# Optimization experiments

Hardware: AMD Instinct MI355X
Metric: run time of the kernel (lower is better)

The kernel has to match this reference:

```python
import jax, jax.numpy as jnp
import numpy as np

B, S, H = 32, 512, 768
NHEAD, DH = 8, 96          # 8 heads * 96 = 768
E = 4096                   # edges per sample
NC = 2
NEG = -1e9
EPS = 1e-5


def _p(k, shape, scale=0.02):
    return scale * jax.random.normal(k, shape, dtype=jnp.float32)


def setup_inputs() -> dict:
    key = jax.random.key(0)
    ks = jax.random.split(key, 24)
    z = lambda *s: jnp.zeros(s, jnp.float32)
    return {
        "diff_encoded": jax.random.normal(ks[0], (B, S, H), jnp.float32),
        "msg_encoded": jax.random.normal(ks[1], (B, S, H), jnp.float32),
        "msg_mask": jnp.ones((B, S), jnp.int32),
        "edge_index_diff": jax.random.randint(ks[2], (B, 2, E), 0, S),
        "edge_index_msg": jax.random.randint(ks[3], (B, 2, E), 0, S),
        # GATv2Conv(heads=1): lin_l (source/message), lin_r (target), att vector, output bias
        "gat_wl": _p(ks[4], (H, H)), "gat_bl": z(H),
        "gat_wr": _p(ks[5], (H, H)), "gat_br": z(H),
        "gat_att": _p(ks[6], (H,)), "gat_bias": z(H),
        # cross MultiheadAttention
        "wq": _p(ks[7], (H, H)), "bq": z(H),
        "wk": _p(ks[8], (H, H)), "bk": z(H),
        "wv": _p(ks[9], (H, H)), "bv": z(H),
        "wo": _p(ks[10], (H, H)), "bo": z(H),
        # LayerNorm + MLP head
        "ln_g": jnp.ones((H,), jnp.float32), "ln_b": z(H),
        "fc0_w": _p(ks[11], (H, 512)), "fc0_b": z(512),
        "fc1_w": _p(ks[12], (512, 128)), "fc1_b": z(128),
        "fc2_w": _p(ks[13], (128, NC)), "fc2_b": z(NC),
    }


def _gat_single(x, edges, wl, bl, wr, br, att, bias):
    # GATv2Conv, heads=1, add_self_loops=True. x: [N,H], edges: [2,E] (src, dst).
    N = x.shape[0]
    src, dst = edges[0], edges[1]
    valid = (src < N) & (dst < N)            # clip_edge_index, as a mask
    src = jnp.where(valid, src, 0)
    dst = jnp.where(valid, dst, 0)
    loop = jnp.arange(N, dtype=src.dtype)    # PyG adds self loops
    src_a = jnp.concatenate([src, loop])
    dst_a = jnp.concatenate([dst, loop])
    valid_a = jnp.concatenate([valid, jnp.ones((N,), bool)])
    xl = x @ wl + bl                          # source / message transform
    xr = x @ wr + br                          # target transform
    e = jax.nn.leaky_relu(xl[src_a] + xr[dst_a], 0.2) @ att   # [E+N]
    e = jnp.where(valid_a, e, NEG)
    emax = jax.ops.segment_max(e, dst_a, num_segments=N)
    p = jnp.exp(e - emax[dst_a]) * valid_a.astype(x.dtype)
    denom = jax.ops.segment_sum(p, dst_a, num_segments=N)
    alpha = p / denom[dst_a]
    out = jax.ops.segment_sum(alpha[:, None] * xl[src_a], dst_a, num_segments=N)
    return out + bias


_gat = jax.vmap(_gat_single, in_axes=(0, 0) + (None,) * 6)


def _layernorm(x, g, b):
    mu = jnp.mean(x, -1, keepdims=True)
    var = jnp.mean(jnp.square(x - mu), -1, keepdims=True)
    return (x - mu) * jax.lax.rsqrt(var + EPS) * g + b


def reference(diff_encoded, msg_encoded, msg_mask, edge_index_diff, edge_index_msg,
              gat_wl, gat_bl, gat_wr, gat_br, gat_att, gat_bias,
              wq, bq, wk, bk, wv, bv, wo, bo, ln_g, ln_b,
              fc0_w, fc0_b, fc1_w, fc1_b, fc2_w, fc2_b):
    diff_g = _gat(diff_encoded, edge_index_diff, gat_wl, gat_bl, gat_wr, gat_br, gat_att, gat_bias) + diff_encoded
    msg_g = _gat(msg_encoded, edge_index_msg, gat_wl, gat_bl, gat_wr, gat_br, gat_att, gat_bias) + msg_encoded
    # cross attention: query=diff_g, key/value=msg_g, key_padding_mask = (msg_mask == 0)
    q = (diff_g @ wq + bq).reshape(B, S, NHEAD, DH)
    k = (msg_g @ wk + bk).reshape(B, S, NHEAD, DH)
    v = (msg_g @ wv + bv).reshape(B, S, NHEAD, DH)
    scores = jnp.einsum("bqhd,bkhd->bhqk", q, k) / jnp.sqrt(jnp.float32(DH))
    scores = jnp.where((msg_mask == 0)[:, None, None, :], NEG, scores)
    attn = jax.nn.softmax(scores, axis=-1)
    ctx = jnp.einsum("bhqk,bkhd->bqhd", attn, v).reshape(B, S, H) @ wo + bo
    fused = _layernorm(ctx + diff_g, ln_g, ln_b)
    x = fused[:, 0, :]                                  # CLS token
    x = jax.nn.relu(x @ fc0_w + fc0_b)                  # dropout = identity (eval)
    x = jax.nn.relu(x @ fc1_w + fc1_b)
    return x @ fc2_w + fc2_b
```

## Files before the change

### kernel.cpp

```cpp
#include <hip/hip_runtime.h>
#include <hip/hip_bf16.h>
#include <math.h>

#define BB 32
#define SS 512
#define HH 768
#define NHEADC 8
#define DHC 96
#define EE 4096
#define NCC 2
#define CAPC 128
#define CAP2 32
#define GSL 36
#define NEGV -1000000000.0f
#define EPSV 1e-5f

#define PREP_CVT  12288
#define PREP_WT   2304
#define PREP_BIAS 3
#define PREP_CNT  512
#define PREP_TOT  (PREP_CVT + PREP_WT + PREP_BIAS + PREP_CNT)

typedef __hip_bfloat16 bf16;
typedef __bf16 bf16x8 __attribute__((ext_vector_type(8)));
typedef float f32x4 __attribute__((ext_vector_type(4)));

static __device__ inline unsigned short f2bf_u(float f) {
  __hip_bfloat16 h = __float2bfloat16(f);
  return *(unsigned short*)&h;
}
static __device__ inline float bfu(unsigned short u) {
  return __uint_as_float(((unsigned int)u) << 16);
}
static __device__ inline float bf2f(bf16 h) { return __bfloat162float(h); }

static __device__ inline void gload16(const void* g, void* l) {
  __builtin_amdgcn_global_load_lds(
      (const __attribute__((address_space(1))) void*)g,
      (__attribute__((address_space(3))) void*)l, 16, 0, 0);
}

__global__ __launch_bounds__(256) void k_prep(
    const float* __restrict__ msg_enc, bf16* __restrict__ Abf,
    const float* __restrict__ gat_wl, const float* __restrict__ gat_wr,
    const float* __restrict__ wk, const float* __restrict__ wv,
    bf16* __restrict__ wtA, bf16* __restrict__ wtB,
    const float* __restrict__ gat_bl, const float* __restrict__ gat_br,
    const float* __restrict__ bk, const float* __restrict__ bv,
    float* __restrict__ biasA, float* __restrict__ biasB,
    const int* __restrict__ e_diff,
    int* __restrict__ dcnt, int* __restrict__ dsrc)
{
  int blk = blockIdx.x, tid = threadIdx.x;
  if (blk < PREP_CVT) {
    int i = (blk * 256 + tid) * 4;
    float4 v = *(const float4*)(msg_enc + i);
    ushort4 o;
    o.x = f2bf_u(v.x); o.y = f2bf_u(v.y); o.z = f2bf_u(v.z); o.w = f2bf_u(v.w);
    *(ushort4*)((unsigned short*)Abf + i) = o;
    return;
  }
  blk -= PREP_CVT;
  if (blk < PREP_WT) {
    int z = blk / 576, rr = blk - z * 576;
    int bx = rr % 24, by = rr / 24;
    const float* w; bf16* o;
    switch (z) {
      case 0: w = gat_wl; o = wtA; break;
      case 1: w = gat_wr; o = wtA + (size_t)HH * HH; break;
      case 2: w = wk;     o = wtB; break;
      default: w = wv;    o = wtB + (size_t)HH * HH; break;
    }
    __shared__ float t[32][33];
    int n0 = bx * 32, k0 = by * 32;
    int x = tid & 31, y = tid >> 5;
    for (int yy = y; yy < 32; yy += 8)
      t[yy][x] = w[(size_t)(k0 + yy) * HH + n0 + x];
    __syncthreads();
    for (int yy = y; yy < 32; yy += 8)
      o[(size_t)(n0 + yy) * HH + k0 + x] = __float2bfloat16(t[x][yy]);
    return;
  }
  blk -= PREP_WT;
  if (blk < PREP_BIAS) {
    int t = blk * 256 + tid;
    if (t < HH) {
      biasA[t] = gat_bl[t]; biasA[HH + t] = gat_br[t];
      biasB[t] = bk[t];     biasB[HH + t] = bv[t];
    }
    return;
  }
  blk -= PREP_BIAS;
  {
    int i = blk * 256 + tid;
    if (i >= BB * EE) return;
    int b = i / EE, j = i - b * EE;
    int s2 = e_diff[b * 2 * EE + j], d2 = e_diff[b * 2 * EE + EE + j];
    if (s2 >= 0 && s2 < SS && d2 == 0) {
      int pos = atomicAdd(&dcnt[b], 1);
      if (pos < CAPC) dsrc[b * CAPC + pos] = s2;
    }
    if (j == 0) {
      int pos = atomicAdd(&dcnt[b], 1);
      if (pos < CAPC) dsrc[b * CAPC + pos] = 0;
    }
  }
}

__global__ __launch_bounds__(512) void k_bin(
    const int* __restrict__ e_msg, int* __restrict__ cnt,
    int* __restrict__ offs, int* __restrict__ binned)
{
  __shared__ int lc[SS];
  __shared__ int tmp[SS];
  int b = blockIdx.x, t = threadIdx.x;
  lc[t] = 0;
  __syncthreads();
  int ss[8], dd[8];
  #pragma unroll
  for (int r = 0; r < 8; ++r) {
    int j = r * 512 + t;
    ss[r] = e_msg[b * 2 * EE + j];
    dd[r] = e_msg[b * 2 * EE + EE + j];
    if (ss[r] >= 0 && ss[r] < SS && dd[r] >= 0 && dd[r] < SS)
      atomicAdd(&lc[dd[r]], 1);
    else
      dd[r] = -1;
  }
  __syncthreads();
  int x = lc[t];
  tmp[t] = x;
  __syncthreads();
  for (int off = 1; off < SS; off <<= 1) {
    int u = (t >= off) ? tmp[t - off] : 0;
    __syncthreads();
    tmp[t] += u;
    __syncthreads();
  }
  int ex = tmp[t] - x;
  cnt[b * SS + t] = x;
  offs[b * SS + t] = ex;
  __syncthreads();
  lc[t] = ex;
  __syncthreads();
  #pragma unroll
  for (int r = 0; r < 8; ++r) {
    if (dd[r] >= 0) {
      int pos = atomicAdd(&lc[dd[r]], 1);
      binned[(size_t)b * EE + pos] = ss[r];
    }
  }
}

template <typename OT>
__global__ __launch_bounds__(256) void k_gemm(
    const bf16* __restrict__ A, const bf16* __restrict__ Bt,
    const float* __restrict__ bias, OT* __restrict__ C0, OT* __restrict__ C1,
    int M, int K)
{
  __shared__ __align__(16) bf16 As0[128 * 32];
  __shared__ __align__(16) bf16 As1[128 * 32];
  __shared__ __align__(16) bf16 Bs0[128 * 32];
  __shared__ __align__(16) bf16 Bs1[128 * 32];
  const int tid = threadIdx.x;
  const int wv = tid >> 6, lane = tid & 63;
  const int bm = blockIdx.x * 128, bn = blockIdx.y * 128;
  const int wm = (wv & 1) * 64, wn = (wv >> 1) * 64;
  const int m16 = lane & 15, half = lane >> 4;
  f32x4 acc[4][4];
  #pragma unroll
  for (int i = 0; i < 4; ++i)
    #pragma unroll
    for (int j = 0; j < 4; ++j) acc[i][j] = (f32x4){0.f, 0.f, 0.f, 0.f};

  const int c0 = tid, c1 = tid + 256;
  const int r0 = c0 >> 2, o0 = (c0 & 3) * 8;
  const int r1 = c1 >> 2, o1 = (c1 & 3) * 8;
  const size_t aB0 = (size_t)(bm + r0) * K + o0;
  const size_t aB1 = (size_t)(bm + r1) * K + o1;
  const size_t bB0 = (size_t)(bn + r0) * K + o0;
  const size_t bB1 = (size_t)(bn + r1) * K + o1;

  for (int k0 = 0; k0 < K; k0 += 64) {
    __syncthreads();
    gload16(A + aB0 + k0, As0 + (size_t)c0 * 8);
    gload16(A + aB1 + k0, As0 + (size_t)c1 * 8);
    gload16(A + aB0 + k0 + 32, As1 + (size_t)c0 * 8);
    gload16(A + aB1 + k0 + 32, As1 + (size_t)c1 * 8);
    gload16(Bt + bB0 + k0, Bs0 + (size_t)c0 * 8);
    gload16(Bt + bB1 + k0, Bs0 + (size_t)c1 * 8);
    gload16(Bt + bB0 + k0 + 32, Bs1 + (size_t)c0 * 8);
    gload16(Bt + bB1 + k0 + 32, Bs1 + (size_t)c1 * 8);
    __syncthreads();
    #pragma unroll
    for (int ks = 0; ks < 2; ++ks) {
      const bf16* Ah = ks ? As1 : As0;
      const bf16* Bh = ks ? Bs1 : Bs0;
      bf16x8 af[4], bfv[4];
      #pragma unroll
      for (int t = 0; t < 4; ++t) {
        af[t]  = *(const bf16x8*)(Ah + (wm + t * 16 + m16) * 32 + half * 8);
        bfv[t] = *(const bf16x8*)(Bh + (wn + t * 16 + m16) * 32 + half * 8);
      }
      #pragma unroll
      for (int i = 0; i < 4; ++i)
        #pragma unroll
        for (int j = 0; j < 4; ++j)
          acc[i][j] = __builtin_amdgcn_mfma_f32_16x16x32_bf16(af[i], bfv[j], acc[i][j], 0, 0, 0);
    }
  }
  #pragma unroll
  for (int i = 0; i < 4; ++i) {
    #pragma unroll
    for (int j = 0; j < 4; ++j) {
      int col = bn + wn + j * 16 + m16;
      float bv = bias ? bias[col] : 0.f;
      OT* Cb = (col < HH) ? C0 : C1;
      int cc = (col < HH) ? col : col - HH;
      #pragma unroll
      for (int r = 0; r < 4; ++r) {
        int row = bm + wm + i * 16 + half * 4 + r;
        float v = acc[i][j][r] + bv;
        if constexpr (sizeof(OT) == 2)
          Cb[(size_t)row * HH + cc] = (OT)__float2bfloat16(v);
        else
          Cb[(size_t)row * HH + cc] = v;
      }
    }
  }
}

__global__ __launch_bounds__(256, 2) void k_gemm256(
    const bf16* __restrict__ A, const bf16* __restrict__ Bt,
    const float* __restrict__ bias, bf16* __restrict__ C0, bf16* __restrict__ C1)
{
  constexpr int K = 768;
  constexpr int NT = K / 32;
  __shared__ __align__(16) bf16 Asm[3][256 * 32];
  __shared__ __align__(16) bf16 Bsm[3][128 * 32];

  const int tid = threadIdx.x;
  const int wv = tid >> 6, lane = tid & 63;
  const int m16 = lane & 15, half = lane >> 4;

  const int bid = blockIdx.x;
  const int swz = (bid & 7) * 96 + (bid >> 3);
  const int bm = (swz / 12) * 256;
  const int bn = (swz % 12) * 128;

  const int wm = (wv & 1) * 128;
  const int wn = (wv >> 1) * 64;

  size_t srcA[4], srcB[2];
  #pragma unroll
  for (int li = 0; li < 4; ++li) {
    int L = li * 256 + tid;
    int row = L >> 2, s = L & 3;
    int g = s ^ ((row >> 1) & 3);
    srcA[li] = (size_t)(bm + row) * K + g * 8;
  }
  #pragma unroll
  for (int li = 0; li < 2; ++li) {
    int L = li * 256 + tid;
    int row = L >> 2, s = L & 3;
    int g = s ^ ((row >> 1) & 3);
    srcB[li] = (size_t)(bn + row) * K + g * 8;
  }

  auto stage = [&](int t, bf16* ba, bf16* bb) {
    #pragma unroll
    for (int li = 0; li < 4; ++li)
      gload16(A + srcA[li] + (size_t)t * 32, ba + (size_t)(li * 256 + tid) * 8);
    #pragma unroll
    for (int li = 0; li < 2; ++li)
      gload16(Bt + srcB[li] + (size_t)t * 32, bb + (size_t)(li * 256 + tid) * 8);
  };

  f32x4 acc[8][4];
  #pragma unroll
  for (int i = 0; i < 8; ++i)
    #pragma unroll
    for (int j = 0; j < 4; ++j) acc[i][j] = (f32x4){0.f, 0.f, 0.f, 0.f};

  const int xs8 = (half ^ ((m16 >> 1) & 3)) * 8;
  const int aBase = (wm + m16) * 32 + xs8;
  const int bBase = (wn + m16) * 32 + xs8;

  auto tile = [&](const bf16* __restrict__ Ab, const bf16* __restrict__ Bb) {
    bf16x8 af[8], bfv[4];
    #pragma unroll
    for (int j = 0; j < 4; ++j) bfv[j] = *(const bf16x8*)(Bb + bBase + j * 512);
    #pragma unroll
    for (int i = 0; i < 8; ++i) af[i] = *(const bf16x8*)(Ab + aBase + i * 512);
    __builtin_amdgcn_s_setprio(1);
    #pragma unroll
    for (int i = 0; i < 8; ++i)
      #pragma unroll
      for (int j = 0; j < 4; ++j)
        acc[i][j] = __builtin_amdgcn_mfma_f32_16x16x32_bf16(af[i], bfv[j], acc[i][j], 0, 0, 0);
    __builtin_amdgcn_s_setprio(0);
  };

  auto step = [&](int kt, int cur, int nxt) {
    if (kt == NT - 1) asm volatile("s_waitcnt vmcnt(0)" ::: "memory");
    else              asm volatile("s_waitcnt vmcnt(6)" ::: "memory");
    __builtin_amdgcn_s_barrier();
    __builtin_amdgcn_sched_barrier(0);
    if (kt + 2 < NT) stage(kt + 2, Asm[nxt], Bsm[nxt]);
    tile(Asm[cur], Bsm[cur]);
  };

  stage(0, Asm[0], Bsm[0]);
  stage(1, Asm[1], Bsm[1]);
  for (int kt3 = 0; kt3 < NT; kt3 += 3) {
    step(kt3 + 0, 0, 2);
    step(kt3 + 1, 1, 0);
    step(kt3 + 2, 2, 1);
  }

  #pragma unroll
  for (int i = 0; i < 8; ++i) {
    #pragma unroll
    for (int j = 0; j < 4; ++j) {
      int col = bn + wn + j * 16 + m16;
      float bv = bias[col];
      bf16* Cb = (col < HH) ? C0 : C1;
      int cc = (col < HH) ? col : col - HH;
      #pragma unroll
      for (int r = 0; r < 4; ++r) {
        int row = bm + wm + i * 16 + half * 4 + r;
        Cb[(size_t)row * HH + cc] = (bf16)__float2bfloat16(acc[i][j][r] + bv);
      }
    }
  }
}

__global__ __launch_bounds__(256) void k_gat_fused(
    const int* __restrict__ binned, const int* __restrict__ offs,
    const int* __restrict__ cnt, const bf16* __restrict__ xl,
    const bf16* __restrict__ xrb, const float* __restrict__ att,
    const float* __restrict__ gbias, const bf16* __restrict__ resid,
    bf16* __restrict__ out)
{
  int bid = blockIdx.x;
  int xcd = bid & 7, idx = bid >> 3;
  int b = xcd * 4 + (idx >> 7);
  int d = (idx & 127) * 4 + (threadIdx.x >> 6);
  int lane = threadIdx.x & 63;
  int base = offs[b * SS + d], n = cnt[b * SS + d];
  const int* bin = binned + (size_t)b * EE + base;
  float av[12];
  {
    const float4* a4 = (const float4*)att;
    #pragma unroll
    for (int r = 0; r < 3; ++r) {
      float4 t = a4[lane + 64 * r];
      av[4*r] = t.x; av[4*r+1] = t.y; av[4*r+2] = t.z; av[4*r+3] = t.w;
    }
  }
  float xr[12];
  {
    const ushort4* p = (const ushort4*)(xrb + ((size_t)b * SS + d) * HH);
    #pragma unroll
    for (int r = 0; r < 3; ++r) {
      ushort4 v = p[lane + 64 * r];
      xr[4*r] = bfu(v.x); xr[4*r+1] = bfu(v.y); xr[4*r+2] = bfu(v.z); xr[4*r+3] = bfu(v.w);
    }
  }
  float m = -3.0e38f, l = 0.f;
  float acc[12] = {};
  int nn = n + 1;
  ushort4 pre[3];
  {
    const ushort4* p = (const ushort4*)(xl + ((size_t)b * SS + d) * HH);
    pre[0] = p[lane]; pre[1] = p[lane + 64]; pre[2] = p[lane + 128];
  }
  for (int j = 0; j < nn; ++j) {
    ushort4 cur0 = pre[0], cur1 = pre[1], cur2 = pre[2];
    if (j + 1 < nn) {
      int sn = bin[j];
      const ushort4* p = (const ushort4*)(xl + ((size_t)b * SS + sn) * HH);
      pre[0] = p[lane]; pre[1] = p[lane + 64]; pre[2] = p[lane + 128];
    }
    float xs[12];
    xs[0] = bfu(cur0.x); xs[1] = bfu(cur0.y); xs[2]  = bfu(cur0.z); xs[3]  = bfu(cur0.w);
    xs[4] = bfu(cur1.x); xs[5] = bfu(cur1.y); xs[6]  = bfu(cur1.z); xs[7]  = bfu(cur1.w);
    xs[8] = bfu(cur2.x); xs[9] = bfu(cur2.y); xs[10] = bfu(cur2.z); xs[11] = bfu(cur2.w);
    float e = 0.f;
    #pragma unroll
    for (int k = 0; k < 12; ++k) {
      float t = xs[k] + xr[k];
      t = t > 0.f ? t : 0.2f * t;
      e += t * av[k];
    }
    #pragma unroll
    for (int off = 32; off > 0; off >>= 1) e += __shfl_xor(e, off);
    float mn = fmaxf(m, e);
    float so = __expf(m - mn);
    float w  = __expf(e - mn);
    l = l * so + w;
    #pragma unroll
    for (int k = 0; k < 12; ++k) acc[k] = acc[k] * so + w * xs[k];
    m = mn;
  }
  float inv = 1.f / l;
  size_t o = ((size_t)b * SS + d) * HH;
  const float4* gb4 = (const float4*)gbias;
  const ushort4* rs4 = (const ushort4*)(resid + o);
  ushort4* out4 = (ushort4*)(out + o);
  #pragma unroll
  for (int r = 0; r < 3; ++r) {
    int c = lane + 64 * r;
    float4 gg = gb4[c];
    ushort4 rr = rs4[c];
    ushort4 ov;
    ov.x = f2bf_u(acc[4*r+0] * inv + gg.x + bfu(rr.x));
    ov.y = f2bf_u(acc[4*r+1] * inv + gg.y + bfu(rr.y));
    ov.z = f2bf_u(acc[4*r+2] * inv + gg.z + bfu(rr.z));
    ov.w = f2bf_u(acc[4*r+3] * inv + gg.w + bfu(rr.w));
    out4[c] = ov;
  }
}

__global__ __launch_bounds__(192) void k_gather_diff(
    const int* __restrict__ dcnt, const int* __restrict__ dsrc,
    const float* __restrict__ diff_enc, bf16* __restrict__ G)
{
  int b = blockIdx.y, jj = blockIdx.x;
  int n = min(dcnt[b], CAP2);
  int t = threadIdx.x;
  size_t orow = ((size_t)b * GSL + jj) * HH;
  ushort4 o = {0, 0, 0, 0};
  if (jj < n || jj == CAP2) {
    int s = (jj == CAP2) ? 0 : dsrc[b * CAPC + jj];
    float4 v = ((const float4*)(diff_enc + ((size_t)b * SS + s) * HH))[t];
    o.x = f2bf_u(v.x); o.y = f2bf_u(v.y); o.z = f2bf_u(v.z); o.w = f2bf_u(v.w);
  }
  *(ushort4*)((unsigned short*)G + orow + t * 4) = o;
}

__global__ __launch_bounds__(256) void k_diff_gat0(
    const int* __restrict__ dcnt, const float* __restrict__ GDl,
    const float* __restrict__ GDr, const float* __restrict__ att,
    const float* __restrict__ gbias, const float* __restrict__ diff_enc,
    float* __restrict__ dg0)
{
  int b = blockIdx.x;
  int n = min(dcnt[b], CAP2);
  __shared__ float ee[CAP2];
  __shared__ float al[CAP2];
  __shared__ float xr0s[HH];
  int wave = threadIdx.x >> 6, lane = threadIdx.x & 63;
  for (int h = threadIdx.x; h < HH; h += 256)
    xr0s[h] = GDr[((size_t)b * GSL + CAP2) * HH + h];
  __syncthreads();
  for (int jj = wave; jj < n; jj += 4) {
    const float* px = GDl + ((size_t)b * GSL + jj) * HH;
    float part = 0.f;
    #pragma unroll
    for (int r = 0; r < HH / 64; ++r) {
      int h = lane + 64 * r;
      float t = px[h] + xr0s[h];
      t = t > 0.f ? t : 0.2f * t;
      part += t * att[h];
    }
    #pragma unroll
    for (int off = 32; off > 0; off >>= 1) part += __shfl_xor(part, off);
    if (lane == 0) ee[jj] = part;
  }
  __syncthreads();
  if (threadIdx.x == 0) {
    float m = -3.0e38f;
    for (int i = 0; i < n; ++i) m = fmaxf(m, ee[i]);
    float ssum = 0.f;
    for (int i = 0; i < n; ++i) ssum += expf(ee[i] - m);
    float inv = 1.f / ssum;
    for (int i = 0; i < n; ++i) al[i] = expf(ee[i] - m) * inv;
  }
  __syncthreads();
  for (int h = threadIdx.x; h < HH; h += 256) {
    float acc = 0.f;
    for (int i = 0; i < n; ++i) acc += al[i] * GDl[((size_t)b * GSL + i) * HH + h];
    dg0[b * HH + h] = acc + gbias[h] + diff_enc[(size_t)b * SS * HH + h];
  }
}

__global__ __launch_bounds__(256) void k_colmat(
    const float* __restrict__ in, const float* __restrict__ w,
    const float* __restrict__ bias, const float* __restrict__ extra,
    float* __restrict__ outp, int Kd, int Nd, long in_stride, int relu)
{
  int b = blockIdx.y, n0 = blockIdx.x * 64;
  int tid = threadIdx.x, wv = tid >> 6, lane = tid & 63;
  __shared__ float xs[HH];
  __shared__ float red[4][64];
  const float* src = in + (size_t)b * in_stride;
  for (int k = tid; k < Kd; k += 256) xs[k] = src[k];
  __syncthreads();
  int h = n0 + lane;
  int kpw = Kd >> 2;
  int kb = wv * kpw;
  float acc = 0.f;
  for (int k = 0; k < kpw; k += 8) {
    #pragma unroll
    for (int u = 0; u < 8; ++u) {
      int kk = kb + k + u;
      acc += xs[kk] * w[(size_t)kk * Nd + h];
    }
  }
  red[wv][lane] = acc;
  __syncthreads();
  if (tid < 64) {
    float s = red[0][tid] + red[1][tid] + red[2][tid] + red[3][tid] + bias[n0 + tid];
    if (extra) s += extra[(size_t)b * Nd + n0 + tid];
    if (relu) s = fmaxf(s, 0.f);
    outp[(size_t)b * Nd + n0 + tid] = s;
  }
}

__global__ __launch_bounds__(256) void k_lnfc0(
    const float* __restrict__ fpre, const float* __restrict__ g,
    const float* __restrict__ bta,
    const float* __restrict__ fc0w, const float* __restrict__ fc0b,
    float* __restrict__ a0g)
{
  int b = blockIdx.y, n0 = blockIdx.x * 64;
  int tid = threadIdx.x, wv = tid >> 6, lane = tid & 63;
  __shared__ float xs[HH];
  __shared__ float red[4][64];
  __shared__ float rs[4], rq[4];
  float v0 = fpre[b * HH + tid];
  float v1 = fpre[b * HH + tid + 256];
  float v2 = fpre[b * HH + tid + 512];
  float sum = v0 + v1 + v2;
  float sq = v0 * v0 + v1 * v1 + v2 * v2;
  #pragma unroll
  for (int off = 32; off > 0; off >>= 1) { sum += __shfl_xor(sum, off); sq += __shfl_xor(sq, off); }
  if (lane == 0) { rs[wv] = sum; rq[wv] = sq; }
  __syncthreads();
  sum = rs[0] + rs[1] + rs[2] + rs[3];
  sq = rq[0] + rq[1] + rq[2] + rq[3];
  float mu = sum / HH;
  float var = sq / HH - mu * mu;
  float scl = rsqrtf(var + EPSV);
  xs[tid]       = (v0 - mu) * scl * g[tid]       + bta[tid];
  xs[tid + 256] = (v1 - mu) * scl * g[tid + 256] + bta[tid + 256];
  xs[tid + 512] = (v2 - mu) * scl * g[tid + 512] + bta[tid + 512];
  __syncthreads();
  int h = n0 + lane;
  int kb = wv * 192;
  float acc = 0.f;
  for (int k = 0; k < 192; k += 8) {
    #pragma unroll
    for (int u = 0; u < 8; ++u) {
      int kk = kb + k + u;
      acc += xs[kk] * fc0w[(size_t)kk * 512 + h];
    }
  }
  red[wv][lane] = acc;
  __syncthreads();
  if (tid < 64) {
    float s = red[0][tid] + red[1][tid] + red[2][tid] + red[3][tid] + fc0b[n0 + tid];
    a0g[(size_t)b * 512 + n0 + tid] = fmaxf(s, 0.f);
  }
}

__global__ __launch_bounds__(256) void k_fc12(
    const float* __restrict__ a0g, const float* __restrict__ fc1w,
    const float* __restrict__ fc1b, const float* __restrict__ fc2w,
    const float* __restrict__ fc2b, float* __restrict__ out)
{
  int b = blockIdx.x, tid = threadIdx.x;
  __shared__ float a0s[512];
  __shared__ float a1s[128];
  __shared__ float r1[2][128];
  for (int k = tid; k < 512; k += 256) a0s[k] = a0g[b * 512 + k];
  __syncthreads();
  int o = tid & 127, hf = tid >> 7;
  int kb = hf * 256;
  float acc = 0.f;
  for (int k = 0; k < 256; k += 8) {
    #pragma unroll
    for (int u = 0; u < 8; ++u) {
      int kk = kb + k + u;
      acc += a0s[kk] * fc1w[(size_t)kk * 128 + o];
    }
  }
  r1[hf][o] = acc;
  __syncthreads();
  if (tid < 128) a1s[tid] = fmaxf(r1[0][tid] + r1[1][tid] + fc1b[tid], 0.f);
  __syncthreads();
  if (tid < 128) {
    int oo = tid >> 6, l = tid & 63;
    float p = a1s[l] * fc2w[l * 2 + oo] + a1s[l + 64] * fc2w[(l + 64) * 2 + oo];
    #pragma unroll
    for (int off = 32; off > 0; off >>= 1) p += __shfl_xor(p, off);
    if (l == 0) out[b * NCC + oo] = p + fc2b[oo];
  }
}

__global__ __launch_bounds__(512) void k_attn(
    const float* __restrict__ q0, const bf16* __restrict__ kb,
    const bf16* __restrict__ vb, const int* __restrict__ mask,
    float* __restrict__ ctx)
{
  int b = blockIdx.x / NHEADC, hd = blockIdx.x % NHEADC;
  __shared__ float qs[DHC];
  __shared__ float sc[SS];
  __shared__ float redm[8];
  __shared__ float reds[8];
  __shared__ float pr4[4][DHC];
  int tid = threadIdx.x;
  if (tid < DHC) qs[tid] = q0[b * HH + hd * DHC + tid];
  __syncthreads();
  const float scale = 0.10206207261596575f;
  {
    int s = tid;
    const int4* pk4 = (const int4*)(kb + ((size_t)b * SS + s) * HH + hd * DHC);
    float acc = 0.f;
    #pragma unroll
    for (int c = 0; c < 12; ++c) {
      int4 raw = pk4[c];
      const unsigned short* u = (const unsigned short*)&raw;
      #pragma unroll
      for (int j = 0; j < 8; ++j) acc += qs[c * 8 + j] * bfu(u[j]);
    }
    sc[s] = (mask[b * SS + s] != 0) ? acc * scale : NEGV;
  }
  __syncthreads();
  int wave = tid >> 6, lane = tid & 63;
  float m = sc[tid];
  #pragma unroll
  for (int off = 32; off > 0; off >>= 1) m = fmaxf(m, __shfl_xor(m, off));
  if (lane == 0) redm[wave] = m;
  __syncthreads();
  m = redm[0];
  #pragma unroll
  for (int i = 1; i < 8; ++i) m = fmaxf(m, redm[i]);
  float p0 = expf(sc[tid] - m);
  float ssum = p0;
  #pragma unroll
  for (int off = 32; off > 0; off >>= 1) ssum += __shfl_xor(ssum, off);
  if (lane == 0) reds[wave] = ssum;
  __syncthreads();
  ssum = reds[0] + reds[1] + reds[2] + reds[3] + reds[4] + reds[5] + reds[6] + reds[7];
  float inv = 1.f / ssum;
  sc[tid] = p0 * inv;
  __syncthreads();
  {
    int hs = tid >> 7, d = tid & 127;
    if (d < DHC) {
      const bf16* pv = vb + ((size_t)b * SS + hs * 128) * HH + hd * DHC + d;
      float acc = 0.f;
      for (int s = 0; s < 128; s += 8) {
        #pragma unroll
        for (int u = 0; u < 8; ++u)
          acc += sc[hs * 128 + s + u] * bf2f(pv[(size_t)(s + u) * HH]);
      }
      pr4[hs][d] = acc;
    }
  }
  __syncthreads();
  if (tid < DHC)
    ctx[b * HH + hd * DHC + tid] = pr4[0][tid] + pr4[1][tid] + pr4[2][tid] + pr4[3][tid];
}

extern "C" void kernel_launch(void* const* d_in, const int* in_sizes, int n_in,
                              void* d_out, int out_size, void* d_ws, size_t ws_size,
                              hipStream_t stream) {
  const float* diff_enc = (const float*)d_in[0];
  const float* msg_enc  = (const float*)d_in[1];
  const int*   msg_mask = (const int*)d_in[2];
  const int*   e_diff   = (const int*)d_in[3];
  const int*   e_msg    = (const int*)d_in[4];
  const float* gat_wl   = (const float*)d_in[5];
  const float* gat_bl   = (const float*)d_in[6];
  const float* gat_wr   = (const float*)d_in[7];
  const float* gat_br   = (const float*)d_in[8];
  const float* gat_att  = (const float*)d_in[9];
  const float* gat_bias = (const float*)d_in[10];
  const float* wq = (const float*)d_in[11];
  const float* bq = (const float*)d_in[12];
  const float* wk = (const float*)d_in[13];
  const float* bk = (const float*)d_in[14];
  const float* wv = (const float*)d_in[15];
  const float* bv = (const float*)d_in[16];
  const float* wo = (const float*)d_in[17];
  const float* bo = (const float*)d_in[18];
  const float* ln_g = (const float*)d_in[19];
  const float* ln_b = (const float*)d_in[20];
  const float* fc0w = (const float*)d_in[21];
  const float* fc0b = (const float*)d_in[22];
  const float* fc1w = (const float*)d_in[23];
  const float* fc1b = (const float*)d_in[24];
  const float* fc2w = (const float*)d_in[25];
  const float* fc2b = (const float*)d_in[26];
  float* out = (float*)d_out;

  char* ws = (char*)d_ws;
  size_t off = 0;
  auto alloc = [&](size_t bytes) -> void* {
    void* p = (void*)(ws + off);
    off += (bytes + 255) & ~(size_t)255;
    return p;
  };
  bf16* Abf    = (bf16*)alloc((size_t)BB * SS * HH * 2);
  bf16* xl     = (bf16*)alloc((size_t)BB * SS * HH * 2);
  bf16* xrb    = (bf16*)alloc((size_t)BB * SS * HH * 2);
  bf16* kbuf   = (bf16*)alloc((size_t)BB * SS * HH * 2);
  bf16* vbuf   = (bf16*)alloc((size_t)BB * SS * HH * 2);
  bf16* mg     = (bf16*)alloc((size_t)BB * SS * HH * 2);
  bf16* wtA    = (bf16*)alloc((size_t)2 * HH * HH * 2);
  bf16* wtB    = (bf16*)alloc((size_t)2 * HH * HH * 2);
  float* biasA = (float*)alloc((size_t)2 * HH * 4);
  float* biasB = (float*)alloc((size_t)2 * HH * 4);
  int*   cnt   = (int*)alloc((size_t)BB * SS * 4);
  int*   offs  = (int*)alloc((size_t)BB * SS * 4);
  int*   binned= (int*)alloc((size_t)BB * EE * 4);
  bf16*  G     = (bf16*)alloc((size_t)BB * GSL * HH * 2);
  float* GDl   = (float*)alloc((size_t)BB * GSL * HH * 4);
  float* GDr   = (float*)alloc((size_t)BB * GSL * HH * 4);
  int*   dcnt  = (int*)alloc((size_t)BB * 4);
  int*   dsrc  = (int*)alloc((size_t)BB * CAPC * 4);
  float* dg0   = (float*)alloc((size_t)BB * HH * 4);
  float* q0    = (float*)alloc((size_t)BB * HH * 4);
  float* ctx   = (float*)alloc((size_t)BB * HH * 4);
  float* fpre  = (float*)alloc((size_t)BB * HH * 4);
  float* a0g   = (float*)alloc((size_t)BB * 512 * 4);

  hipMemsetAsync(dcnt, 0, (size_t)BB * 4, stream);

  k_prep<<<PREP_TOT, 256, 0, stream>>>(msg_enc, Abf, gat_wl, gat_wr, wk, wv,
                                       wtA, wtB, gat_bl, gat_br, bk, bv,
                                       biasA, biasB, e_diff, dcnt, dsrc);
  k_bin<<<BB, 512, 0, stream>>>(e_msg, cnt, offs, binned);

  k_gemm256<<<768, 256, 0, stream>>>(Abf, wtA, biasA, xl, xrb);
  k_gat_fused<<<(BB * SS) / 4, 256, 0, stream>>>(binned, offs, cnt, xl, xrb,
                                                 gat_att, gat_bias, Abf, mg);
  k_gemm256<<<768, 256, 0, stream>>>(mg, wtB, biasB, kbuf, vbuf);
  {
    dim3 gBlk(256);
    dim3 gg(GSL, BB);
    k_gather_diff<<<gg, 192, 0, stream>>>(dcnt, dsrc, diff_enc, G);
    dim3 gGridD((BB * GSL) / 128, (2 * HH) / 128);
    k_gemm<float><<<gGridD, gBlk, 0, stream>>>(G, wtA, biasA, GDl, GDr, BB * GSL, HH);
  }
  k_diff_gat0<<<BB, 256, 0, stream>>>(dcnt, GDl, GDr, gat_att, gat_bias, diff_enc, dg0);
  {
    dim3 g(HH / 64, BB);
    k_colmat<<<g, 256, 0, stream>>>(dg0, wq, bq, nullptr, q0, HH, HH, HH, 0);
  }
  k_attn<<<BB * NHEADC, 512, 0, stream>>>(q0, kbuf, vbuf, msg_mask, ctx);
  {
    dim3 g(HH / 64, BB);
    k_colmat<<<g, 256, 0, stream>>>(ctx, wo, bo, dg0, fpre, HH, HH, HH, 0);
  }
  {
    dim3 g(512 / 64, BB);
    k_lnfc0<<<g, 256, 0, stream>>>(fpre, ln_g, ln_b, fc0w, fc0b, a0g);
  }
  k_fc12<<<BB, 256, 0, stream>>>(a0g, fc1w, fc1b, fc2w, fc2b, out);
}
```

Measured before the change: 438.7 us.

## Retile main GEMM to 512 threads with K=64 steps; fuse Q projection into attention

The 256x128 GEMM now runs 8 waves of 64x64 sub-tiles instead of 4 waves of 128x64, with a 64-deep K step and a matching XOR swizzle. Fragment loads are split into four phases interleaved with MFMA groups. This halves the number of k-iterations and barriers and cuts per-thread accumulator registers. The cost is 144KB of LDS, which limits the kernel to one block per CU. Separately, the query projection kernel is removed and its work moved into k_attn, where each head block computes its 96 q values from dg0 and wq. That saves a launch but repeats the dg0 load in every head block.

Measured after the change: 424.6 us. 3.2% less time.

```diff
diff --git a/kernel.cpp b/kernel.cpp
--- a/kernel.cpp
+++ b/kernel.cpp
@@ -230,14 +230,14 @@
   }
 }
 
-__global__ __launch_bounds__(256, 2) void k_gemm256(
+__global__ __launch_bounds__(512) void k_gemm256(
     const bf16* __restrict__ A, const bf16* __restrict__ Bt,
     const float* __restrict__ bias, bf16* __restrict__ C0, bf16* __restrict__ C1)
 {
   constexpr int K = 768;
-  constexpr int NT = K / 32;
-  __shared__ __align__(16) bf16 Asm[3][256 * 32];
-  __shared__ __align__(16) bf16 Bsm[3][128 * 32];
+  constexpr int NT = K / 64;
+  __shared__ __align__(16) bf16 Asm[3][256 * 64];
+  __shared__ __align__(16) bf16 Bsm[3][128 * 64];
 
   const int tid = threadIdx.x;
   const int wv = tid >> 6, lane = tid & 63;
@@ -248,56 +248,87 @@
   const int bm = (swz / 12) * 256;
   const int bn = (swz % 12) * 128;
 
-  const int wm = (wv & 1) * 128;
-  const int wn = (wv >> 1) * 64;
+  const int wm = (wv >> 1) * 64;
+  const int wn = (wv & 1) * 64;
 
   size_t srcA[4], srcB[2];
   #pragma unroll
   for (int li = 0; li < 4; ++li) {
-    int L = li * 256 + tid;
-    int row = L >> 2, s = L & 3;
-    int g = s ^ ((row >> 1) & 3);
+    int L = li * 512 + tid;
+    int row = L >> 3;
+    int g = (L & 7) ^ (row & 7);
     srcA[li] = (size_t)(bm + row) * K + g * 8;
   }
   #pragma unroll
   for (int li = 0; li < 2; ++li) {
-    int L = li * 256 + tid;
-    int row = L >> 2, s = L & 3;
-    int g = s ^ ((row >> 1) & 3);
+    int L = li * 512 + tid;
+    int row = L >> 3;
+    int g = (L & 7) ^ (row & 7);
     srcB[li] = (size_t)(bn + row) * K + g * 8;
   }
 
   auto stage = [&](int t, bf16* ba, bf16* bb) {
     #pragma unroll
     for (int li = 0; li < 4; ++li)
-      gload16(A + srcA[li] + (size_t)t * 32, ba + (size_t)(li * 256 + tid) * 8);
+      gload16(A + srcA[li] + (size_t)t * 64, ba + (size_t)(li * 512 + tid) * 8);
     #pragma unroll
     for (int li = 0; li < 2; ++li)
-      gload16(Bt + srcB[li] + (size_t)t * 32, bb + (size_t)(li * 256 + tid) * 8);
+      gload16(Bt + srcB[li] + (size_t)t * 64, bb + (size_t)(li * 512 + tid) * 8);
   };
 
-  f32x4 acc[8][4];
-  #pragma unroll
-  for (int i = 0; i < 8; ++i)
+  f32x4 acc[4][4];
+  #pragma unroll
+  for (int i = 0; i < 4; ++i)
     #pragma unroll
     for (int j = 0; j < 4; ++j) acc[i][j] = (f32x4){0.f, 0.f, 0.f, 0.f};
 
-  const int xs8 = (half ^ ((m16 >> 1) & 3)) * 8;
-  const int aBase = (wm + m16) * 32 + xs8;
-  const int bBase = (wn + m16) * 32 + xs8;
+  const int xr = m16 & 7;
+  const int aoff0 = (wm + m16) * 64 + ((half ^ xr) * 8);
+  const int aoff1 = (wm + m16) * 64 + (((4 + half) ^ xr) * 8);
+  const int boff0 = (wn + m16) * 64 + ((half ^ xr) * 8);
+  const int boff1 = (wn + m16) * 64 + (((4 + half) ^ xr) * 8);
 
   auto tile = [&](const bf16* __restrict__ Ab, const bf16* __restrict__ Bb) {
-    bf16x8 af[8], bfv[4];
-    #pragma unroll
-    for (int j = 0; j < 4; ++j) bfv[j] = *(const bf16x8*)(Bb + bBase + j * 512);
-    #pragma unroll
-    for (int i = 0; i < 8; ++i) af[i] = *(const bf16x8*)(Ab + aBase + i * 512);
+    bf16x8 b0[4], b1[4], a0[2], a1[2], a2[2], a3[2];
+    #pragma unroll
+    for (int j = 0; j < 4; ++j) b0[j] = *(const bf16x8*)(Bb + boff0 + j * 1024);
+    #pragma unroll
+    for (int i = 0; i < 2; ++i) a0[i] = *(const bf16x8*)(Ab + aoff0 + i * 1024);
     __builtin_amdgcn_s_setprio(1);
     #pragma unroll
-    for (int i = 0; i < 8; ++i)
+    for (int i = 0; i < 2; ++i)
       #pragma unroll
       for (int j = 0; j < 4; ++j)
-        acc[i][j] = __builtin_amdgcn_mfma_f32_16x16x32_bf16(af[i], bfv[j], acc[i][j], 0, 0, 0);
+        acc[i][j] = __builtin_amdgcn_mfma_f32_16x16x32_bf16(a0[i], b0[j], acc[i][j], 0, 0, 0);
+    __builtin_amdgcn_s_setprio(0);
+    #pragma unroll
+    for (int i = 0; i < 2; ++i) a1[i] = *(const bf16x8*)(Ab + aoff0 + (i + 2) * 1024);
+    __builtin_amdgcn_s_setprio(1);
+    #pragma unroll
+    for (int i = 0; i < 2; ++i)
+      #pragma unroll
+      for (int j = 0; j < 4; ++j)
+        acc[i + 2][j] = __builtin_amdgcn_mfma_f32_16x16x32_bf16(a1[i], b0[j], acc[i + 2][j], 0, 0, 0);
+    __builtin_amdgcn_s_setprio(0);
+    #pragma unroll
+    for (int j = 0; j < 4; ++j) b1[j] = *(const bf16x8*)(Bb + boff1 + j * 1024);
+    #pragma unroll
+    for (int i = 0; i < 2; ++i) a2[i] = *(const bf16x8*)(Ab + aoff1 + i * 1024);
+    __builtin_amdgcn_s_setprio(1);
+    #pragma unroll
+    for (int i = 0; i < 2; ++i)
+      #pragma unroll
+      for (int j = 0; j < 4; ++j)
+        acc[i][j] = __builtin_amdgcn_mfma_f32_16x16x32_bf16(a2[i], b1[j], acc[i][j], 0, 0, 0);
+    __builtin_amdgcn_s_setprio(0);
+    #pragma unroll
+    for (int i = 0; i < 2; ++i) a3[i] = *(const bf16x8*)(Ab + aoff1 + (i + 2) * 1024);
+    __builtin_amdgcn_s_setprio(1);
+    #pragma unroll
+    for (int i = 0; i < 2; ++i)
+      #pragma unroll
+      for (int j = 0; j < 4; ++j)
+        acc[i + 2][j] = __builtin_amdgcn_mfma_f32_16x16x32_bf16(a3[i], b1[j], acc[i + 2][j], 0, 0, 0);
     __builtin_amdgcn_s_setprio(0);
   };
 
@@ -319,7 +350,7 @@
   }
 
   #pragma unroll
-  for (int i = 0; i < 8; ++i) {
+  for (int i = 0; i < 4; ++i) {
     #pragma unroll
     for (int j = 0; j < 4; ++j) {
       int col = bn + wn + j * 16 + m16;
@@ -600,18 +631,35 @@
 }
 
 __global__ __launch_bounds__(512) void k_attn(
-    const float* __restrict__ q0, const bf16* __restrict__ kb,
+    const float* __restrict__ dg0, const float* __restrict__ wq,
+    const float* __restrict__ bq, const bf16* __restrict__ kb,
     const bf16* __restrict__ vb, const int* __restrict__ mask,
     float* __restrict__ ctx)
 {
   int b = blockIdx.x / NHEADC, hd = blockIdx.x % NHEADC;
+  __shared__ float xg[HH];
   __shared__ float qs[DHC];
   __shared__ float sc[SS];
   __shared__ float redm[8];
   __shared__ float reds[8];
   __shared__ float pr4[4][DHC];
   int tid = threadIdx.x;
-  if (tid < DHC) qs[tid] = q0[b * HH + hd * DHC + tid];
+  for (int k = tid; k < HH; k += 512) xg[k] = dg0[b * HH + k];
+  __syncthreads();
+  if (tid < 384) {
+    int d = tid >> 2, q = tid & 3;
+    const float* wcol = wq + (size_t)(hd * DHC + d);
+    float p = 0.f;
+    int k0 = q * 192;
+    for (int k = 0; k < 192; k += 8) {
+      #pragma unroll
+      for (int u = 0; u < 8; ++u)
+        p += xg[k0 + k + u] * wcol[(size_t)(k0 + k + u) * HH];
+    }
+    p += __shfl_xor(p, 1);
+    p += __shfl_xor(p, 2);
+    if (q == 0) qs[d] = p + bq[hd * DHC + d];
+  }
   __syncthreads();
   const float scale = 0.10206207261596575f;
   {
@@ -723,7 +771,6 @@
   int*   dcnt  = (int*)alloc((size_t)BB * 4);
   int*   dsrc  = (int*)alloc((size_t)BB * CAPC * 4);
   float* dg0   = (float*)alloc((size_t)BB * HH * 4);
-  float* q0    = (float*)alloc((size_t)BB * HH * 4);
   float* ctx   = (float*)alloc((size_t)BB * HH * 4);
   float* fpre  = (float*)alloc((size_t)BB * HH * 4);
   float* a0g   = (float*)alloc((size_t)BB * 512 * 4);
@@ -735,10 +782,10 @@
                                        biasA, biasB, e_diff, dcnt, dsrc);
   k_bin<<<BB, 512, 0, stream>>>(e_msg, cnt, offs, binned);
 
-  k_gemm256<<<768, 256, 0, stream>>>(Abf, wtA, biasA, xl, xrb);
+  k_gemm256<<<768, 512, 0, stream>>>(Abf, wtA, biasA, xl, xrb);
   k_gat_fused<<<(BB * SS) / 4, 256, 0, stream>>>(binned, offs, cnt, xl, xrb,
                                                  gat_att, gat_bias, Abf, mg);
-  k_gemm256<<<768, 256, 0, stream>>>(mg, wtB, biasB, kbuf, vbuf);
+  k_gemm256<<<768, 512, 0, stream>>>(mg, wtB, biasB, kbuf, vbuf);
   {
     dim3 gBlk(256);
     dim3 gg(GSL, BB);
@@ -747,11 +794,7 @@
     k_gemm<float><<<gGridD, gBlk, 0, stream>>>(G, wtA, biasA, GDl, GDr, BB * GSL, HH);
   }
   k_diff_gat0<<<BB, 256, 0, stream>>>(dcnt, GDl, GDr, gat_att, gat_bias, diff_enc, dg0);
-  {
-    dim3 g(HH / 64, BB);
-    k_colmat<<<g, 256, 0, stream>>>(dg0, wq, bq, nullptr, q0, HH, HH, HH, 0);
-  }
-  k_attn<<<BB * NHEADC, 512, 0, stream>>>(q0, kbuf, vbuf, msg_mask, ctx);
+  k_attn<<<BB * NHEADC, 512, 0, stream>>>(dg0, wq, bq, kbuf, vbuf, msg_mask, ctx);
   {
     dim3 g(HH / 64, BB);
     k_colmat<<<g, 256, 0, stream>>>(ctx, wo, bo, dg0, fpre, HH, HH, HH, 0);
```
